# Optimization experiments

Measured on AMD Instinct MI355X. Metric: run time of the kernel, lower is better.

Reference implementation:

```python
import jax, jax.numpy as jnp
import numpy as np

B, N, D, U, S = 32, 1024, 2, 64, 2


def setup_inputs() -> dict:
    key = jax.random.key(0)
    ks = jax.random.split(key, 8)
    scale = 1.0 / np.sqrt(N)  # keep diffusion outputs in a sane range
    inputs = jax.random.normal(ks[0], (B, N, D), jnp.float32)
    supports = jax.random.normal(ks[1], (B, N, N, S), jnp.float32) * scale
    h_prev = jax.random.normal(ks[2], (B, N * U), jnp.float32)
    rows = (D + U) * (S + 1)  # 198
    wscale = 1.0 / np.sqrt(rows)
    r_kernel = jax.random.normal(ks[3], (rows, U), jnp.float32) * wscale
    u_kernel = jax.random.normal(ks[4], (rows, U), jnp.float32) * wscale
    c_kernel = jax.random.normal(ks[5], (rows, U), jnp.float32) * wscale
    zeros = jnp.zeros((U,), jnp.float32)
    return {"inputs": inputs, "supports": supports, "h_prev": h_prev,
            "r_kernel": r_kernel, "r_bias": zeros,
            "u_kernel": u_kernel, "u_bias": zeros,
            "c_kernel": c_kernel, "c_bias": zeros}


def _diff_conv(x_in, supports, state, kernel, bias):
    # x_in: (B,N,D), state: (B, N*U) -> output (B, N*U)
    b, n, _ = x_in.shape
    u = kernel.shape[1]
    x0 = jnp.concatenate([x_in, state.reshape(b, n, u)], axis=-1)  # (B,N,F)
    # batched graph diffusion for all S supports at once: (B,N,N,S)x(B,N,F)->(B,N,F,S)
    xm = jnp.einsum('bijs,bjf->bifs', supports, x0)
    x = jnp.concatenate([x0[..., None], xm], axis=-1)  # (B,N,F,M) matches tf stack+transpose order
    x = x.reshape(b * n, -1) @ kernel + bias  # (B*N, U)
    return x.reshape(b, n * u)


def reference(inputs, supports, h_prev, r_kernel, r_bias, u_kernel, u_bias, c_kernel, c_bias):
    r = jax.nn.sigmoid(_diff_conv(inputs, supports, h_prev, r_kernel, r_bias))
    u = jax.nn.sigmoid(_diff_conv(inputs, supports, h_prev, u_kernel, u_bias))
    c = jnp.tanh(_diff_conv(inputs, supports, r * h_prev, c_kernel, c_bias))
    h = u * h_prev + (1.0 - u) * c
    return h
```

## Files before the change

### kernel.cpp

```cpp
#include <hip/hip_runtime.h>
#include <hip/hip_bf16.h>

namespace {

constexpr int kN  = 1024;
constexpr int kU  = 64;
constexpr int kFP = 80;
constexpr int kXR = 132;

typedef __attribute__((ext_vector_type(4))) float f32x4;
typedef __attribute__((ext_vector_type(8))) short sv8;
typedef unsigned int u32;

__device__ __forceinline__ unsigned pack_bf2(float a, float b) {
  __hip_bfloat16 ha = __float2bfloat16(a);
  __hip_bfloat16 hb = __float2bfloat16(b);
  unsigned short ua = *reinterpret_cast<unsigned short*>(&ha);
  unsigned short ub = *reinterpret_cast<unsigned short*>(&hb);
  return (unsigned)ua | ((unsigned)ub << 16);
}

__device__ __forceinline__ void gl16(const void* g, void* l) {
  __builtin_amdgcn_global_load_lds(
      (const __attribute__((address_space(1))) u32*)g,
      (__attribute__((address_space(3))) u32*)l, 16, 0, 0);
}

__global__ __launch_bounds__(256) void build_x0t(
    const float* __restrict__ inputs, const float* __restrict__ h_prev,
    __hip_bfloat16* __restrict__ x0t, __hip_bfloat16* __restrict__ x0tc) {
  const int bx = blockIdx.x;
  const int b  = bx >> 4;
  const int n0 = (bx & 15) * 64;
  const int t  = threadIdx.x;

  __shared__ float hp[64][65];

  const float* hpg = h_prev + (size_t)b * kN * kU + (size_t)n0 * kU;
#pragma unroll
  for (int r = 0; r < 16; ++r) {
    int idx = t + (r << 8);
    hp[idx >> 6][idx & 63] = hpg[idx];
  }
  __syncthreads();

  {
    int u = t >> 2, g = t & 3;
    __hip_bfloat16* dst = x0t + ((size_t)b * kFP + 2 + u) * kN + n0 + g * 16;
#pragma unroll
    for (int k = 0; k < 16; ++k) dst[k] = __float2bfloat16(hp[g * 16 + k][u]);
  }

  if (t < 128) {
    int d = t & 1, nn = t >> 1;
    float v = inputs[((size_t)b * kN + n0 + nn) * 2 + d];
    __hip_bfloat16 bv = __float2bfloat16(v);
    x0t [((size_t)b * kFP + d) * kN + n0 + nn] = bv;
    x0tc[((size_t)b * kFP + d) * kN + n0 + nn] = bv;
  } else {
    int i2 = t - 128;
    __hip_bfloat16 z = __float2bfloat16(0.0f);
#pragma unroll
    for (int r = 0; r < 7; ++r) {
      int idx = i2 + r * 128;
      int row = 66 + (idx >> 6), nn = idx & 63;
      x0t [((size_t)b * kFP + row) * kN + n0 + nn] = z;
      x0tc[((size_t)b * kFP + row) * kN + n0 + nn] = z;
    }
  }
}

__global__ __launch_bounds__(256, 4) void einsum_diff(
    const float* __restrict__ sup, const __hip_bfloat16* __restrict__ x0t,
    float* __restrict__ xfeat) {
  const int bx   = blockIdx.x;
  const int b    = bx >> 5;
  const int i0   = (bx & 31) << 5;
  const int t    = threadIdx.x;
  const int lane = t & 63;
  const int w    = t >> 6;
  const int q    = lane >> 4;
  const int lm   = lane & 15;
  const int s    = w & 1;
  const int ih   = w >> 1;

  __shared__ unsigned short Xf[2][10][64][8];
  __shared__ unsigned short Af[2][2][2][2][64][8];

  f32x4 acc[5];
#pragma unroll
  for (int n = 0; n < 5; ++n) acc[n] = (f32x4){0.f, 0.f, 0.f, 0.f};

  const float* sbase = sup + ((size_t)b * kN + i0) * (kN * 2);
  const unsigned short* xg =
      reinterpret_cast<const unsigned short*>(x0t) + (size_t)b * kFP * kN;

  const float* aB[4];
#pragma unroll
  for (int r = 0; r < 4; ++r) {
    int fl = t + (r << 8);
    int ii = fl >> 5, cc = fl & 31;
    aB[r] = sbase + (size_t)ii * (kN * 2) + cc * 4;
  }

  const unsigned short* xsA;
  const unsigned short* xsB;
  const unsigned short* xsC;
  {
    int segA = w;
    int segB = w + 4;
    int segC = w + 8;
    int ksA = segA / 5, nA = segA % 5;
    int ksB = segB / 5, nB = segB % 5;
    int ksC = segC / 5, nC = segC % 5;
    xsA = xg + (size_t)(nA * 16 + lm) * kN + ksA * 32 + q * 8;
    xsB = xg + (size_t)(nB * 16 + lm) * kN + ksB * 32 + q * 8;
    xsC = xg + (size_t)(nC * 16 + lm) * kN + ksC * 32 + q * 8;
  }

  auto dmaX = [&](int nb, int T) {
    int jo = T * 64;
    gl16(xsA + jo, &Xf[nb][w][0][0]);
    gl16(xsB + jo, &Xf[nb][w + 4][0][0]);
    if (w < 2) gl16(xsC + jo, &Xf[nb][w + 8][0][0]);
  };

  auto loadA = [&](float4 (&R)[4], int T) {
    int jo2 = T * 128;
#pragma unroll
    for (int r = 0; r < 4; ++r)
      R[r] = *reinterpret_cast<const float4*>(aB[r] + jo2);
  };

  auto repack = [&](const float4 (&cur)[4], int nb) {
#pragma unroll
    for (int r = 0; r < 4; ++r) {
      int fl = t + (r << 8);
      int ii = fl >> 5, cc = fl & 31;
      int ks = cc >> 4, cb2 = cc & 15;
      int q2 = cb2 >> 2, e = (cb2 & 3) * 2;
      int lane2 = q2 * 16 + (ii & 15);
      int ihh = ii >> 4;
      float4 v = cur[r];
      *reinterpret_cast<u32*>(&Af[nb][0][ks][ihh][lane2][e]) = pack_bf2(v.x, v.z);
      *reinterpret_cast<u32*>(&Af[nb][1][ks][ihh][lane2][e]) = pack_bf2(v.y, v.w);
    }
  };

  auto compute = [&](int cb_) {
#pragma unroll
    for (int ks = 0; ks < 2; ++ks) {
      sv8 a = *reinterpret_cast<const sv8*>(&Af[cb_][s][ks][ih][lane][0]);
#pragma unroll
      for (int n = 0; n < 5; ++n) {
        sv8 xb = *reinterpret_cast<const sv8*>(&Xf[cb_][ks * 5 + n][lane][0]);
        acc[n] = __builtin_amdgcn_mfma_f32_16x16x32_bf16(a, xb, acc[n], 0, 0, 0);
      }
    }
  };

  float4 P[4], Q[4];

  dmaX(0, 0);
  loadA(P, 0);
  asm volatile("s_waitcnt vmcnt(0)" ::: "memory");
  repack(P, 0);
  loadA(P, 1);
  asm volatile("s_waitcnt lgkmcnt(0)" ::: "memory");
  __builtin_amdgcn_s_barrier();
  __builtin_amdgcn_sched_barrier(0);

#define BODY(T, CUR, NXT, ISSUE)                                      \
  {                                                                   \
    const int nb_ = ((T) + 1) & 1;                                    \
    dmaX(nb_, (T) + 1);                                               \
    if (ISSUE) loadA(NXT, (T) + 2);                                   \
    compute((T) & 1);                                                 \
    if (ISSUE) { asm volatile("s_waitcnt vmcnt(4)" ::: "memory"); }   \
    else       { asm volatile("s_waitcnt vmcnt(0)" ::: "memory"); }   \
    repack(CUR, nb_);                                                 \
    asm volatile("s_waitcnt lgkmcnt(0)" ::: "memory");                \
    __builtin_amdgcn_s_barrier();                                     \
    __builtin_amdgcn_sched_barrier(0);                                \
  }

#pragma unroll 1
  for (int t2 = 0; t2 < 7; ++t2) {
    int tt = t2 * 2;
    BODY(tt,     P, Q, true);
    BODY(tt + 1, Q, P, true);
  }
  BODY(14, P, Q, false);
  compute(1);
#undef BODY

  size_t rbase = ((size_t)(b * kN) + i0 + ih * 16 + q * 4) * kXR + s * 66;
#pragma unroll
  for (int n = 0; n < 5; ++n) {
    int f = n * 16 + lm;
    if (f < 66) {
#pragma unroll
      for (int r = 0; r < 4; ++r)
        xfeat[rbase + (size_t)r * kXR + f] = acc[n][r];
    }
  }
}

__global__ __launch_bounds__(256) void gates_ru(
    const float* __restrict__ xfeat, const float* __restrict__ rk,
    const float* __restrict__ rbias, const float* __restrict__ uk,
    const float* __restrict__ ubias, const float* __restrict__ inputs,
    const float* __restrict__ h_prev, float* __restrict__ u_buf,
    __hip_bfloat16* __restrict__ x0tc) {
  const int row0 = blockIdx.x * 32;
  const int b = row0 >> 10, n0 = row0 & 1023;
  const int t = threadIdx.x;
  __shared__ float xm[32][132];
  __shared__ float x0s[32][66];

  {
    const float4* xsrc = reinterpret_cast<const float4*>(xfeat + (size_t)row0 * kXR);
    float4* xdst = reinterpret_cast<float4*>(&xm[0][0]);
#pragma unroll
    for (int r2 = 0; r2 < 5; ++r2) {
      int fl = t + (r2 << 8);
      if (fl < 1056) xdst[fl] = xsrc[fl];
    }
  }
#pragma unroll
  for (int r2 = 0; r2 < 8; ++r2) {
    int idx = t + (r2 << 8);
    int rw = idx >> 6, u = idx & 63;
    x0s[rw][2 + u] = h_prev[(size_t)(row0 + rw) * kU + u];
  }
  if (t < 64) x0s[t >> 1][t & 1] = inputs[(size_t)row0 * 2 + t];
  __syncthreads();

  const int cu = t & 15;
  const int rw = (t >> 4) * 2;
  float ar[2][4] = {{0.f,0.f,0.f,0.f},{0.f,0.f,0.f,0.f}};
  float au[2][4] = {{0.f,0.f,0.f,0.f},{0.f,0.f,0.f,0.f}};

#pragma unroll 4
  for (int f = 0; f < 66; ++f) {
    float4 vr = *reinterpret_cast<const float4*>(rk + (size_t)(f * 3) * kU + cu * 4);
    float4 vu = *reinterpret_cast<const float4*>(uk + (size_t)(f * 3) * kU + cu * 4);
    float a0 = x0s[rw][f], a1 = x0s[rw + 1][f];
    ar[0][0] += a0 * vr.x; ar[0][1] += a0 * vr.y; ar[0][2] += a0 * vr.z; ar[0][3] += a0 * vr.w;
    ar[1][0] += a1 * vr.x; ar[1][1] += a1 * vr.y; ar[1][2] += a1 * vr.z; ar[1][3] += a1 * vr.w;
    au[0][0] += a0 * vu.x; au[0][1] += a0 * vu.y; au[0][2] += a0 * vu.z; au[0][3] += a0 * vu.w;
    au[1][0] += a1 * vu.x; au[1][1] += a1 * vu.y; au[1][2] += a1 * vu.z; au[1][3] += a1 * vu.w;
  }
#pragma unroll
  for (int m = 1; m <= 2; ++m) {
#pragma unroll 4
    for (int f = 0; f < 66; ++f) {
      float4 vr = *reinterpret_cast<const float4*>(rk + (size_t)(f * 3 + m) * kU + cu * 4);
      float4 vu = *reinterpret_cast<const float4*>(uk + (size_t)(f * 3 + m) * kU + cu * 4);
      float a0 = xm[rw][(m - 1) * 66 + f], a1 = xm[rw + 1][(m - 1) * 66 + f];
      ar[0][0] += a0 * vr.x; ar[0][1] += a0 * vr.y; ar[0][2] += a0 * vr.z; ar[0][3] += a0 * vr.w;
      ar[1][0] += a1 * vr.x; ar[1][1] += a1 * vr.y; ar[1][2] += a1 * vr.z; ar[1][3] += a1 * vr.w;
      au[0][0] += a0 * vu.x; au[0][1] += a0 * vu.y; au[0][2] += a0 * vu.z; au[0][3] += a0 * vu.w;
      au[1][0] += a1 * vu.x; au[1][1] += a1 * vu.y; au[1][2] += a1 * vu.z; au[1][3] += a1 * vu.w;
    }
  }

#pragma unroll
  for (int rr = 0; rr < 2; ++rr) {
    int grow = row0 + rw + rr;
    int n = n0 + rw + rr;
#pragma unroll
    for (int j = 0; j < 4; ++j) {
      int u = cu * 4 + j;
      float rv = 1.f / (1.f + __expf(-(ar[rr][j] + rbias[u])));
      float uv = 1.f / (1.f + __expf(-(au[rr][j] + ubias[u])));
      u_buf[(size_t)grow * kU + u] = uv;
      float rh = rv * h_prev[(size_t)grow * kU + u];
      x0tc[((size_t)b * kFP + 2 + u) * kN + n] = __float2bfloat16(rh);
    }
  }
}

__global__ __launch_bounds__(256) void gate_c_final(
    const float* __restrict__ xfeat, const float* __restrict__ ck,
    const float* __restrict__ cbias, const float* __restrict__ inputs,
    const __hip_bfloat16* __restrict__ x0tc, const float* __restrict__ h_prev,
    const float* __restrict__ u_buf, float* __restrict__ out) {
  const int row0 = blockIdx.x * 32;
  const int b = row0 >> 10, n0 = row0 & 1023;
  const int t = threadIdx.x;
  __shared__ float xm[32][132];
  __shared__ float x0c[32][66];

  {
    const float4* xsrc = reinterpret_cast<const float4*>(xfeat + (size_t)row0 * kXR);
    float4* xdst = reinterpret_cast<float4*>(&xm[0][0]);
#pragma unroll
    for (int r2 = 0; r2 < 5; ++r2) {
      int fl = t + (r2 << 8);
      if (fl < 1056) xdst[fl] = xsrc[fl];
    }
  }
#pragma unroll
  for (int r2 = 0; r2 < 8; ++r2) {
    int idx = t + (r2 << 8);
    int u = idx >> 5, nn = idx & 31;
    x0c[nn][2 + u] =
        __bfloat162float(x0tc[((size_t)b * kFP + 2 + u) * kN + n0 + nn]);
  }
  if (t < 64) x0c[t >> 1][t & 1] = inputs[(size_t)row0 * 2 + t];
  __syncthreads();

  const int cu = t & 15;
  const int rw = (t >> 4) * 2;
  float ac[2][4] = {{0.f,0.f,0.f,0.f},{0.f,0.f,0.f,0.f}};

#pragma unroll 4
  for (int f = 0; f < 66; ++f) {
    float4 vc = *reinterpret_cast<const float4*>(ck + (size_t)(f * 3) * kU + cu * 4);
    float a0 = x0c[rw][f], a1 = x0c[rw + 1][f];
    ac[0][0] += a0 * vc.x; ac[0][1] += a0 * vc.y; ac[0][2] += a0 * vc.z; ac[0][3] += a0 * vc.w;
    ac[1][0] += a1 * vc.x; ac[1][1] += a1 * vc.y; ac[1][2] += a1 * vc.z; ac[1][3] += a1 * vc.w;
  }
#pragma unroll
  for (int m = 1; m <= 2; ++m) {
#pragma unroll 4
    for (int f = 0; f < 66; ++f) {
      float4 vc = *reinterpret_cast<const float4*>(ck + (size_t)(f * 3 + m) * kU + cu * 4);
      float a0 = xm[rw][(m - 1) * 66 + f], a1 = xm[rw + 1][(m - 1) * 66 + f];
      ac[0][0] += a0 * vc.x; ac[0][1] += a0 * vc.y; ac[0][2] += a0 * vc.z; ac[0][3] += a0 * vc.w;
      ac[1][0] += a1 * vc.x; ac[1][1] += a1 * vc.y; ac[1][2] += a1 * vc.z; ac[1][3] += a1 * vc.w;
    }
  }

#pragma unroll
  for (int rr = 0; rr < 2; ++rr) {
    int grow = row0 + rw + rr;
#pragma unroll
    for (int j = 0; j < 4; ++j) {
      int u = cu * 4 + j;
      float cv = tanhf(ac[rr][j] + cbias[u]);
      float uv = u_buf[(size_t)grow * kU + u];
      float hp = h_prev[(size_t)grow * kU + u];
      out[(size_t)grow * kU + u] = uv * hp + (1.f - uv) * cv;
    }
  }
}

}

extern "C" void kernel_launch(void* const* d_in, const int* in_sizes, int n_in,
                              void* d_out, int out_size, void* d_ws, size_t ws_size,
                              hipStream_t stream) {
  const float* inputs = (const float*)d_in[0];
  const float* sup    = (const float*)d_in[1];
  const float* h_prev = (const float*)d_in[2];
  const float* rk     = (const float*)d_in[3];
  const float* rbias  = (const float*)d_in[4];
  const float* uk     = (const float*)d_in[5];
  const float* ubias  = (const float*)d_in[6];
  const float* ck     = (const float*)d_in[7];
  const float* cbias  = (const float*)d_in[8];
  float* out = (float*)d_out;

  char* ws = (char*)d_ws;
  __hip_bfloat16* x0t   = (__hip_bfloat16*)(ws);
  __hip_bfloat16* x0tc  = (__hip_bfloat16*)(ws + 5242880);
  float*          xfeat = (float*)(ws + 10485760);
  float*          u_buf = (float*)(ws + 27787264);

  hipLaunchKernelGGL(build_x0t, dim3(512), dim3(256), 0, stream,
                     inputs, h_prev, x0t, x0tc);
  hipLaunchKernelGGL(einsum_diff, dim3(1024), dim3(256), 0, stream,
                     sup, x0t, xfeat);
  hipLaunchKernelGGL(gates_ru, dim3(1024), dim3(256), 0, stream,
                     xfeat, rk, rbias, uk, ubias, inputs, h_prev, u_buf, x0tc);
  hipLaunchKernelGGL(einsum_diff, dim3(1024), dim3(256), 0, stream,
                     sup, x0tc, xfeat);
  hipLaunchKernelGGL(gate_c_final, dim3(1024), dim3(256), 0, stream,
                     xfeat, ck, cbias, inputs, x0tc, h_prev, u_buf, out);
}
```

Before: 253.6 us.

## Enlarge einsum tiles, swizzle LDS, store diffusion features as bf16

The einsum kernel now uses 512-thread blocks, each covering 64 output rows, with a remapped block order. Each thread loads 64 contiguous bytes of the support tensor and writes them to LDS through an XOR-swizzled layout with 16-byte stores. The A double-buffering shrinks to a single register set with a full vmcnt wait. The diffusion features are staged through LDS and written as packed bf16, and the gate kernels unpack them, halving that intermediate traffic. The costs are lower precision in the intermediate features and less latency hiding on the support loads.

```diff
diff --git a/kernel.cpp b/kernel.cpp
--- a/kernel.cpp
+++ b/kernel.cpp
@@ -11,13 +11,28 @@
 typedef __attribute__((ext_vector_type(4))) float f32x4;
 typedef __attribute__((ext_vector_type(8))) short sv8;
 typedef unsigned int u32;
-
-__device__ __forceinline__ unsigned pack_bf2(float a, float b) {
+typedef unsigned short u16;
+
+__device__ __forceinline__ u32 pack_bf2(float a, float b) {
   __hip_bfloat16 ha = __float2bfloat16(a);
   __hip_bfloat16 hb = __float2bfloat16(b);
-  unsigned short ua = *reinterpret_cast<unsigned short*>(&ha);
-  unsigned short ub = *reinterpret_cast<unsigned short*>(&hb);
-  return (unsigned)ua | ((unsigned)ub << 16);
+  u16 ua = *reinterpret_cast<u16*>(&ha);
+  u16 ub = *reinterpret_cast<u16*>(&hb);
+  return (u32)ua | ((u32)ub << 16);
+}
+
+__device__ __forceinline__ u16 bf16bits(float a) {
+  __hip_bfloat16 h = __float2bfloat16(a);
+  return *reinterpret_cast<u16*>(&h);
+}
+
+__device__ __forceinline__ float bflo(u32 v) {
+  u32 x = v << 16;
+  return *reinterpret_cast<float*>(&x);
+}
+__device__ __forceinline__ float bfhi(u32 v) {
+  u32 x = v & 0xffff0000u;
+  return *reinterpret_cast<float*>(&x);
 }
 
 __device__ __forceinline__ void gl16(const void* g, void* l) {
@@ -70,12 +85,13 @@
   }
 }
 
-__global__ __launch_bounds__(256, 4) void einsum_diff(
+__global__ __launch_bounds__(512, 4) void einsum_diff(
     const float* __restrict__ sup, const __hip_bfloat16* __restrict__ x0t,
-    float* __restrict__ xfeat) {
-  const int bx   = blockIdx.x;
-  const int b    = bx >> 5;
-  const int i0   = (bx & 31) << 5;
+    u16* __restrict__ xfeat) {
+  const int bx = blockIdx.x;
+  const int wk = (bx & 7) * 64 + (bx >> 3);
+  const int b  = wk >> 4;
+  const int i0 = (wk & 15) << 6;
   const int t    = threadIdx.x;
   const int lane = t & 63;
   const int w    = t >> 6;
@@ -84,73 +100,71 @@
   const int s    = w & 1;
   const int ih   = w >> 1;
 
-  __shared__ unsigned short Xf[2][10][64][8];
-  __shared__ unsigned short Af[2][2][2][2][64][8];
+  __shared__ u16 Af[2][2][2][4][64][8];
+  __shared__ u16 Xf[2][10][64][8];
 
   f32x4 acc[5];
 #pragma unroll
   for (int n = 0; n < 5; ++n) acc[n] = (f32x4){0.f, 0.f, 0.f, 0.f};
 
   const float* sbase = sup + ((size_t)b * kN + i0) * (kN * 2);
-  const unsigned short* xg =
-      reinterpret_cast<const unsigned short*>(x0t) + (size_t)b * kFP * kN;
-
-  const float* aB[4];
-#pragma unroll
-  for (int r = 0; r < 4; ++r) {
-    int fl = t + (r << 8);
-    int ii = fl >> 5, cc = fl & 31;
-    aB[r] = sbase + (size_t)ii * (kN * 2) + cc * 4;
-  }
-
-  const unsigned short* xsA;
-  const unsigned short* xsB;
-  const unsigned short* xsC;
+  const u16* xg = reinterpret_cast<const u16*>(x0t) + (size_t)b * kFP * kN;
+
+  const int ii = t >> 3, jb = t & 7;
+  const float* aSrc = sbase + (size_t)ii * (kN * 2) + jb * 16;
+  const int ksA = jb >> 2, q2 = jb & 3;
+  const int ihhA = ii >> 4, lm2 = ii & 15;
+  const int aOff = ksA * 4096 + ihhA * 1024 +
+                   ((((q2 * 16 + lm2) * 16)) ^ (q2 << 4) ^ (ksA << 6));
+  char* const afBase = (char*)&Af[0][0][0][0][0][0];
+
+  const int seg1 = w;
+  const int seg2 = w + 8;
+  const u16* xs1;
+  const u16* xs2 = nullptr;
   {
-    int segA = w;
-    int segB = w + 4;
-    int segC = w + 8;
-    int ksA = segA / 5, nA = segA % 5;
-    int ksB = segB / 5, nB = segB % 5;
-    int ksC = segC / 5, nC = segC % 5;
-    xsA = xg + (size_t)(nA * 16 + lm) * kN + ksA * 32 + q * 8;
-    xsB = xg + (size_t)(nB * 16 + lm) * kN + ksB * 32 + q * 8;
-    xsC = xg + (size_t)(nC * 16 + lm) * kN + ksC * 32 + q * 8;
-  }
+    int k1 = seg1 / 5, n1 = seg1 % 5;
+    xs1 = xg + (size_t)(n1 * 16 + lm) * kN + k1 * 32 + q * 8;
+    if (w < 2) {
+      int k2 = seg2 / 5, n2 = seg2 % 5;
+      xs2 = xg + (size_t)(n2 * 16 + lm) * kN + k2 * 32 + q * 8;
+    }
+  }
+
+  float4 R[4];
 
   auto dmaX = [&](int nb, int T) {
     int jo = T * 64;
-    gl16(xsA + jo, &Xf[nb][w][0][0]);
-    gl16(xsB + jo, &Xf[nb][w + 4][0][0]);
-    if (w < 2) gl16(xsC + jo, &Xf[nb][w + 8][0][0]);
+    gl16(xs1 + jo, &Xf[nb][seg1][0][0]);
+    if (w < 2) gl16(xs2 + jo, &Xf[nb][seg2][0][0]);
   };
 
-  auto loadA = [&](float4 (&R)[4], int T) {
-    int jo2 = T * 128;
-#pragma unroll
-    for (int r = 0; r < 4; ++r)
-      R[r] = *reinterpret_cast<const float4*>(aB[r] + jo2);
+  auto loadA = [&](int T) {
+    const float* p = aSrc + T * 128;
+    R[0] = *reinterpret_cast<const float4*>(p);
+    R[1] = *reinterpret_cast<const float4*>(p + 4);
+    R[2] = *reinterpret_cast<const float4*>(p + 8);
+    R[3] = *reinterpret_cast<const float4*>(p + 12);
   };
 
-  auto repack = [&](const float4 (&cur)[4], int nb) {
+  auto packWrite = [&](int nb) {
+    u32 p0[4], p1[4];
 #pragma unroll
     for (int r = 0; r < 4; ++r) {
-      int fl = t + (r << 8);
-      int ii = fl >> 5, cc = fl & 31;
-      int ks = cc >> 4, cb2 = cc & 15;
-      int q2 = cb2 >> 2, e = (cb2 & 3) * 2;
-      int lane2 = q2 * 16 + (ii & 15);
-      int ihh = ii >> 4;
-      float4 v = cur[r];
-      *reinterpret_cast<u32*>(&Af[nb][0][ks][ihh][lane2][e]) = pack_bf2(v.x, v.z);
-      *reinterpret_cast<u32*>(&Af[nb][1][ks][ihh][lane2][e]) = pack_bf2(v.y, v.w);
-    }
+      p0[r] = pack_bf2(R[r].x, R[r].z);
+      p1[r] = pack_bf2(R[r].y, R[r].w);
+    }
+    char* base = afBase + nb * 16384 + aOff;
+    *reinterpret_cast<uint4*>(base)        = *reinterpret_cast<uint4*>(p0);
+    *reinterpret_cast<uint4*>(base + 8192) = *reinterpret_cast<uint4*>(p1);
   };
 
   auto compute = [&](int cb_) {
 #pragma unroll
     for (int ks = 0; ks < 2; ++ks) {
-      sv8 a = *reinterpret_cast<const sv8*>(&Af[cb_][s][ks][ih][lane][0]);
+      const char* ab = afBase + cb_ * 16384 + s * 8192 + ks * 4096 + ih * 1024;
+      sv8 a = *reinterpret_cast<const sv8*>(
+          ab + ((((q * 16 + lm) * 16)) ^ (q << 4) ^ (ks << 6)));
 #pragma unroll
       for (int n = 0; n < 5; ++n) {
         sv8 xb = *reinterpret_cast<const sv8*>(&Xf[cb_][ks * 5 + n][lane][0]);
@@ -159,55 +173,53 @@
     }
   };
 
-  float4 P[4], Q[4];
-
   dmaX(0, 0);
-  loadA(P, 0);
+  loadA(0);
   asm volatile("s_waitcnt vmcnt(0)" ::: "memory");
-  repack(P, 0);
-  loadA(P, 1);
+  packWrite(0);
   asm volatile("s_waitcnt lgkmcnt(0)" ::: "memory");
   __builtin_amdgcn_s_barrier();
   __builtin_amdgcn_sched_barrier(0);
 
-#define BODY(T, CUR, NXT, ISSUE)                                      \
-  {                                                                   \
-    const int nb_ = ((T) + 1) & 1;                                    \
-    dmaX(nb_, (T) + 1);                                               \
-    if (ISSUE) loadA(NXT, (T) + 2);                                   \
-    compute((T) & 1);                                                 \
-    if (ISSUE) { asm volatile("s_waitcnt vmcnt(4)" ::: "memory"); }   \
-    else       { asm volatile("s_waitcnt vmcnt(0)" ::: "memory"); }   \
-    repack(CUR, nb_);                                                 \
-    asm volatile("s_waitcnt lgkmcnt(0)" ::: "memory");                \
-    __builtin_amdgcn_s_barrier();                                     \
-    __builtin_amdgcn_sched_barrier(0);                                \
-  }
-
 #pragma unroll 1
-  for (int t2 = 0; t2 < 7; ++t2) {
-    int tt = t2 * 2;
-    BODY(tt,     P, Q, true);
-    BODY(tt + 1, Q, P, true);
-  }
-  BODY(14, P, Q, false);
+  for (int T = 0; T < 15; ++T) {
+    const int nb = (T + 1) & 1;
+    dmaX(nb, T + 1);
+    loadA(T + 1);
+    compute(T & 1);
+    asm volatile("s_waitcnt vmcnt(0)" ::: "memory");
+    packWrite(nb);
+    asm volatile("s_waitcnt lgkmcnt(0)" ::: "memory");
+    __builtin_amdgcn_s_barrier();
+    __builtin_amdgcn_sched_barrier(0);
+  }
   compute(1);
-#undef BODY
-
-  size_t rbase = ((size_t)(b * kN) + i0 + ih * 16 + q * 4) * kXR + s * 66;
+  __syncthreads();
+
+  u16* ep = (u16*)afBase;
 #pragma unroll
   for (int n = 0; n < 5; ++n) {
     int f = n * 16 + lm;
     if (f < 66) {
 #pragma unroll
-      for (int r = 0; r < 4; ++r)
-        xfeat[rbase + (size_t)r * kXR + f] = acc[n][r];
-    }
+      for (int r = 0; r < 4; ++r) {
+        int row = ih * 16 + q * 4 + r;
+        ep[row * 136 + s * 66 + f] = bf16bits(acc[n][r]);
+      }
+    }
+  }
+  __syncthreads();
+  const u32* ep32 = (const u32*)afBase;
+  u32* og = reinterpret_cast<u32*>(xfeat) + ((size_t)b * kN + i0) * 66;
+#pragma unroll 1
+  for (int g = t; g < 4224; g += 512) {
+    int row = g / 66, c = g - row * 66;
+    og[g] = ep32[row * 68 + c];
   }
 }
 
 __global__ __launch_bounds__(256) void gates_ru(
-    const float* __restrict__ xfeat, const float* __restrict__ rk,
+    const u16* __restrict__ xfeat, const float* __restrict__ rk,
     const float* __restrict__ rbias, const float* __restrict__ uk,
     const float* __restrict__ ubias, const float* __restrict__ inputs,
     const float* __restrict__ h_prev, float* __restrict__ u_buf,
@@ -215,16 +227,17 @@
   const int row0 = blockIdx.x * 32;
   const int b = row0 >> 10, n0 = row0 & 1023;
   const int t = threadIdx.x;
-  __shared__ float xm[32][132];
+  __shared__ float xm[32][134];
   __shared__ float x0s[32][66];
 
   {
-    const float4* xsrc = reinterpret_cast<const float4*>(xfeat + (size_t)row0 * kXR);
-    float4* xdst = reinterpret_cast<float4*>(&xm[0][0]);
-#pragma unroll
-    for (int r2 = 0; r2 < 5; ++r2) {
-      int fl = t + (r2 << 8);
-      if (fl < 1056) xdst[fl] = xsrc[fl];
+    const u32* xsrc = reinterpret_cast<const u32*>(xfeat) + (size_t)row0 * 66;
+#pragma unroll 1
+    for (int g = t; g < 2112; g += 256) {
+      int row = g / 66, c = g - row * 66;
+      u32 v = xsrc[g];
+      xm[row][c * 2]     = bflo(v);
+      xm[row][c * 2 + 1] = bfhi(v);
     }
   }
 #pragma unroll
@@ -282,23 +295,24 @@
 }
 
 __global__ __launch_bounds__(256) void gate_c_final(
-    const float* __restrict__ xfeat, const float* __restrict__ ck,
+    const u16* __restrict__ xfeat, const float* __restrict__ ck,
     const float* __restrict__ cbias, const float* __restrict__ inputs,
     const __hip_bfloat16* __restrict__ x0tc, const float* __restrict__ h_prev,
     const float* __restrict__ u_buf, float* __restrict__ out) {
   const int row0 = blockIdx.x * 32;
   const int b = row0 >> 10, n0 = row0 & 1023;
   const int t = threadIdx.x;
-  __shared__ float xm[32][132];
+  __shared__ float xm[32][134];
   __shared__ float x0c[32][66];
 
   {
-    const float4* xsrc = reinterpret_cast<const float4*>(xfeat + (size_t)row0 * kXR);
-    float4* xdst = reinterpret_cast<float4*>(&xm[0][0]);
-#pragma unroll
-    for (int r2 = 0; r2 < 5; ++r2) {
-      int fl = t + (r2 << 8);
-      if (fl < 1056) xdst[fl] = xsrc[fl];
+    const u32* xsrc = reinterpret_cast<const u32*>(xfeat) + (size_t)row0 * 66;
+#pragma unroll 1
+    for (int g = t; g < 2112; g += 256) {
+      int row = g / 66, c = g - row * 66;
+      u32 v = xsrc[g];
+      xm[row][c * 2]     = bflo(v);
+      xm[row][c * 2 + 1] = bfhi(v);
     }
   }
 #pragma unroll
@@ -366,16 +380,16 @@
   char* ws = (char*)d_ws;
   __hip_bfloat16* x0t   = (__hip_bfloat16*)(ws);
   __hip_bfloat16* x0tc  = (__hip_bfloat16*)(ws + 5242880);
-  float*          xfeat = (float*)(ws + 10485760);
-  float*          u_buf = (float*)(ws + 27787264);
+  u16*            xfeat = (u16*)(ws + 10485760);
+  float*          u_buf = (float*)(ws + 19136512);
 
   hipLaunchKernelGGL(build_x0t, dim3(512), dim3(256), 0, stream,
                      inputs, h_prev, x0t, x0tc);
-  hipLaunchKernelGGL(einsum_diff, dim3(1024), dim3(256), 0, stream,
+  hipLaunchKernelGGL(einsum_diff, dim3(512), dim3(512), 0, stream,
                      sup, x0t, xfeat);
   hipLaunchKernelGGL(gates_ru, dim3(1024), dim3(256), 0, stream,
                      xfeat, rk, rbias, uk, ubias, inputs, h_prev, u_buf, x0tc);
-  hipLaunchKernelGGL(einsum_diff, dim3(1024), dim3(256), 0, stream,
+  hipLaunchKernelGGL(einsum_diff, dim3(512), dim3(512), 0, stream,
                      sup, x0tc, xfeat);
   hipLaunchKernelGGL(gate_c_final, dim3(1024), dim3(256), 0, stream,
                      xfeat, ck, cbias, inputs, x0tc, h_prev, u_buf, out);
```

Measured after the change: 232.6 us. -8.3%, faster.
